# Kernel optimization log

Hardware: AMD Instinct MI355X
Metric: run time of the kernel (lower is better)

Reference implementation:

```python
import jax, jax.numpy as jnp
import numpy as np

N_NODES = 20000
N_EDGES = 640000
NODE_FEATURES = 8
PERIODS = 12
HIDDEN = 32


def _gcn_conv(x, src, dst, dinv, W, b):
    # GCNConv with added self-loops and symmetric normalization:
    # out = D^{-1/2}(A+I)D^{-1/2} (x W) + b
    xw = x @ W                                  # [N, H]
    norm = dinv[src] * dinv[dst]                # [E]
    agg = jax.ops.segment_sum(xw[src] * norm[:, None], dst, num_segments=x.shape[0])
    agg = agg + (dinv * dinv)[:, None] * xw     # self-loop contribution
    return agg + b


def _tgcn_cell(xt, src, dst, dinv, H, W_z, b_z, L_z, lb_z, W_r, b_r, L_r, lb_r, W_h, b_h, L_h, lb_h):
    # TGCN GRU-style cell (torch_geometric_temporal):
    Z = jax.nn.sigmoid(jnp.concatenate([_gcn_conv(xt, src, dst, dinv, W_z, b_z), H], axis=1) @ L_z + lb_z)
    R = jax.nn.sigmoid(jnp.concatenate([_gcn_conv(xt, src, dst, dinv, W_r, b_r), H], axis=1) @ L_r + lb_r)
    H_tilde = jnp.tanh(jnp.concatenate([_gcn_conv(xt, src, dst, dinv, W_h, b_h), H * R], axis=1) @ L_h + lb_h)
    return Z * H + (1.0 - Z) * H_tilde


def setup_inputs() -> dict:
    key = jax.random.key(0)
    ks = jax.random.split(key, 20)
    F, H, P = NODE_FEATURES, HIDDEN, PERIODS
    s = 0.1
    f32 = jnp.float32
    inp = {
        "x": jax.random.normal(ks[0], (N_NODES, F, P), f32),
        "edge_index": jax.random.randint(ks[1], (2, N_EDGES), 0, N_NODES, jnp.int32),
        # GCN gate conv weights (in_channels=F -> out_channels=H)
        "W_z": jax.random.normal(ks[2], (F, H), f32) * s, "b_z": jnp.zeros((H,), f32),
        "W_r": jax.random.normal(ks[3], (F, H), f32) * s, "b_r": jnp.zeros((H,), f32),
        "W_h": jax.random.normal(ks[4], (F, H), f32) * s, "b_h": jnp.zeros((H,), f32),
        # GRU linear layers: Linear(2H, H), stored as [2H, H]
        "L_z": jax.random.normal(ks[5], (2 * H, H), f32) * s, "lb_z": jnp.zeros((H,), f32),
        "L_r": jax.random.normal(ks[6], (2 * H, H), f32) * s, "lb_r": jnp.zeros((H,), f32),
        "L_h": jax.random.normal(ks[7], (2 * H, H), f32) * s, "lb_h": jnp.zeros((H,), f32),
        # attention over periods + final readout Linear(H, P)
        "attention": jax.random.uniform(ks[8], (P,), f32),
        "lin_W": jax.random.normal(ks[9], (H, P), f32) * s,
        "lin_b": jnp.zeros((P,), f32),
    }
    return inp


def reference(x, edge_index, W_z, b_z, W_r, b_r, W_h, b_h,
              L_z, lb_z, L_r, lb_r, L_h, lb_h, attention, lin_W, lin_b):
    N = x.shape[0]
    src, dst = edge_index[0], edge_index[1]
    # symmetric GCN normalization degrees (with self-loops)
    deg = jax.ops.segment_sum(jnp.ones((src.shape[0],), x.dtype), dst, num_segments=N) + 1.0
    dinv = jax.lax.rsqrt(deg)

    probs = jax.nn.softmax(attention)           # [P]
    H0 = jnp.zeros((N, W_z.shape[1]), x.dtype)  # A3TGCN passes H=None each period -> zeros
    xp = jnp.moveaxis(x, -1, 0)                 # [P, N, F]

    def step(acc, pt):
        xt, p = pt
        Hn = _tgcn_cell(xt, src, dst, dinv, H0,
                        W_z, b_z, L_z, lb_z, W_r, b_r, L_r, lb_r, W_h, b_h, L_h, lb_h)
        return acc + p * Hn, None

    H_accum, _ = jax.lax.scan(step, H0, (xp, probs))
    h = jax.nn.relu(H_accum)
    return h @ lin_W + lin_b                    # [N, P]
```

## Files before the change

### kernel.cpp

```cpp
#include <hip/hip_runtime.h>
#include <math.h>

#define NN 20000
#define NE 640000
#define FDIM 8
#define PDIM 12
#define HDIM 32
#define FP 96
#define CAP 96
#define CSTR 16

typedef _Float16 half4v __attribute__((ext_vector_type(4)));
typedef _Float16 half8v __attribute__((ext_vector_type(8)));

__global__ __launch_bounds__(256) void k_prep(
        int* __restrict__ cursor,
        const float* __restrict__ Wz, const float* __restrict__ bz,
        const float* __restrict__ Wh, const float* __restrict__ bh,
        const float* __restrict__ Lz, const float* __restrict__ lbz,
        const float* __restrict__ Lh, const float* __restrict__ lbh,
        const float* __restrict__ att,
        float* __restrict__ Mz, float* __restrict__ Mh,
        float* __restrict__ cz, float* __restrict__ ch,
        float* __restrict__ probs) {
    int tid = blockIdx.x * 256 + threadIdx.x;
    if (tid < NN * CSTR / 4) reinterpret_cast<int4*>(cursor)[tid] = make_int4(0, 0, 0, 0);

    if (blockIdx.x == 0) {
        int t = threadIdx.x;
        int f = t >> 5, h = t & 31;
        float mz = 0.f, mh = 0.f;
        for (int k = 0; k < HDIM; ++k) {
            mz += Wz[f * HDIM + k] * Lz[k * HDIM + h];
            mh += Wh[f * HDIM + k] * Lh[k * HDIM + h];
        }
        Mz[f * HDIM + h] = mz;
        Mh[f * HDIM + h] = mh;
        if (f == 0) {
            float a = lbz[h], b2 = lbh[h];
            for (int k = 0; k < HDIM; ++k) {
                a  += bz[k] * Lz[k * HDIM + h];
                b2 += bh[k] * Lh[k * HDIM + h];
            }
            cz[h] = a; ch[h] = b2;
        }
        if (t == 0) {
            float m = -1e30f;
            for (int p = 0; p < PDIM; ++p) m = fmaxf(m, att[p]);
            float e[PDIM]; float ss = 0.f;
            for (int p = 0; p < PDIM; ++p) { e[p] = expf(att[p] - m); ss += e[p]; }
            for (int p = 0; p < PDIM; ++p) probs[p] = e[p] / ss;
        }
    }
}

__global__ __launch_bounds__(256) void k_bucket(
        const int* __restrict__ src, const int* __restrict__ dst,
        int* __restrict__ cursor, unsigned short* __restrict__ ebuf) {
    int i = blockIdx.x * 256 + threadIdx.x;
    int s = src[i], d = dst[i];
    int p = atomicAdd(&cursor[d * CSTR], 1);
    if (p < CAP) ebuf[d * CAP + p] = (unsigned short)s;
}

__global__ __launch_bounds__(256) void k_xh(const float* __restrict__ x,
                                            const int* __restrict__ cursor,
                                            half8v* __restrict__ xh) {
    int idx = blockIdx.x * 256 + threadIdx.x;
    if (idx >= NN * (FP / 8)) return;
    int node = idx / (FP / 8);
    float dd = rsqrtf((float)cursor[node * CSTR] + 1.0f);
    const float4* xp = reinterpret_cast<const float4*>(x) + (size_t)idx * 2;
    float4 a = xp[0], b = xp[1];
    half8v h;
    h[0] = (_Float16)(dd * a.x); h[1] = (_Float16)(dd * a.y);
    h[2] = (_Float16)(dd * a.z); h[3] = (_Float16)(dd * a.w);
    h[4] = (_Float16)(dd * b.x); h[5] = (_Float16)(dd * b.y);
    h[6] = (_Float16)(dd * b.z); h[7] = (_Float16)(dd * b.w);
    xh[idx] = h;
}

__global__ __launch_bounds__(256) void k_gnode(
        const _Float16* __restrict__ xh, const int* __restrict__ cursor,
        const unsigned short* __restrict__ ebuf,
        const float* __restrict__ Mz, const float* __restrict__ Mh,
        const float* __restrict__ cz, const float* __restrict__ ch,
        const float* __restrict__ probs,
        const float* __restrict__ linW, const float* __restrict__ linb,
        float* __restrict__ out) {
    __shared__ float4 sx4[8 * 24];
    __shared__ float sh[8][HDIM];
    __shared__ float sprobs[PDIM];
    __shared__ unsigned short sle[8 * CAP];
    __shared__ int   scnt[8];
    __shared__ float sdd[8];

    int tid   = threadIdx.x;
    int node0 = blockIdx.x * 8;

    if (tid < PDIM) sprobs[tid] = probs[tid];
    if (tid < 8 * CAP / 4)
        reinterpret_cast<ushort4*>(sle)[tid] =
            reinterpret_cast<const ushort4*>(ebuf + (size_t)node0 * CAP)[tid];
    if (tid < 8) {
        int c = cursor[(node0 + tid) * CSTR];
        scnt[tid] = c < CAP ? c : CAP;
        sdd[tid]  = rsqrtf((float)c + 1.0f);
    }
    __syncthreads();

    int li   = tid >> 5;
    int lane = tid & 31;
    int node = node0 + li;

    if (lane < 24) {
        float dd = sdd[li];
        int e1 = scnt[li];
        const half4v* xh4 = reinterpret_cast<const half4v*>(xh);
        half4v hs = xh4[node * 24 + lane];
        float ax = (float)hs[0], ay = (float)hs[1];
        float az = (float)hs[2], aw = (float)hs[3];
        const unsigned short* eb = &sle[li * CAP];
        int j = 0;
        for (; j + 4 <= e1; j += 4) {
            ushort4 s4 = *reinterpret_cast<const ushort4*>(eb + j);
            half4v a0 = xh4[s4.x * 24 + lane], a1 = xh4[s4.y * 24 + lane];
            half4v a2 = xh4[s4.z * 24 + lane], a3 = xh4[s4.w * 24 + lane];
            ax += ((float)a0[0] + (float)a1[0]) + ((float)a2[0] + (float)a3[0]);
            ay += ((float)a0[1] + (float)a1[1]) + ((float)a2[1] + (float)a3[1]);
            az += ((float)a0[2] + (float)a1[2]) + ((float)a2[2] + (float)a3[2]);
            aw += ((float)a0[3] + (float)a1[3]) + ((float)a2[3] + (float)a3[3]);
        }
        for (; j < e1; ++j) {
            int s = eb[j];
            half4v a = xh4[s * 24 + lane];
            ax += (float)a[0]; ay += (float)a[1]; az += (float)a[2]; aw += (float)a[3];
        }
        float4 o;
        o.x = dd * ax; o.y = dd * ay; o.z = dd * az; o.w = dd * aw;
        sx4[li * 24 + lane] = o;
    }
    __syncthreads();

    int h = lane;
    float rMz[FDIM], rMh[FDIM];
#pragma unroll
    for (int f = 0; f < FDIM; ++f) {
        rMz[f] = Mz[f * HDIM + h];
        rMh[f] = Mh[f * HDIM + h];
    }
    float u[PDIM], v[PDIM];
    float c0 = cz[h], c1 = ch[h];
#pragma unroll
    for (int t = 0; t < PDIM; ++t) { u[t] = c0; v[t] = c1; }

    const float* sxf = reinterpret_cast<const float*>(&sx4[li * 24]);
#pragma unroll
    for (int f = 0; f < FDIM; ++f) {
        const float4 a = *reinterpret_cast<const float4*>(sxf + f * PDIM);
        const float4 b = *reinterpret_cast<const float4*>(sxf + f * PDIM + 4);
        const float4 c = *reinterpret_cast<const float4*>(sxf + f * PDIM + 8);
        float mz = rMz[f], mh = rMh[f];
        u[0] += a.x * mz; u[1]  += a.y * mz; u[2]  += a.z * mz; u[3]  += a.w * mz;
        u[4] += b.x * mz; u[5]  += b.y * mz; u[6]  += b.z * mz; u[7]  += b.w * mz;
        u[8] += c.x * mz; u[9]  += c.y * mz; u[10] += c.z * mz; u[11] += c.w * mz;
        v[0] += a.x * mh; v[1]  += a.y * mh; v[2]  += a.z * mh; v[3]  += a.w * mh;
        v[4] += b.x * mh; v[5]  += b.y * mh; v[6]  += b.z * mh; v[7]  += b.w * mh;
        v[8] += c.x * mh; v[9]  += c.y * mh; v[10] += c.z * mh; v[11] += c.w * mh;
    }

    float accum = 0.f;
#pragma unroll
    for (int t = 0; t < PDIM; ++t) {
        float omz = 1.f / (1.f + __expf(u[t]));
        float th  = 1.f - 2.f / (__expf(2.f * v[t]) + 1.f);
        accum += sprobs[t] * omz * th;
    }
    sh[li][h] = fmaxf(accum, 0.f);
    __builtin_amdgcn_wave_barrier();

    if (h < PDIM) {
        float o = linb[h];
#pragma unroll
        for (int k = 0; k < HDIM; ++k) o += sh[li][k] * linW[k * PDIM + h];
        out[(size_t)node * PDIM + h] = o;
    }
}

static inline size_t al256(size_t x) { return (x + 255) & ~(size_t)255; }

extern "C" void kernel_launch(void* const* d_in, const int* in_sizes, int n_in,
                              void* d_out, int out_size, void* d_ws, size_t ws_size,
                              hipStream_t stream) {
    const float* x    = (const float*)d_in[0];
    const int*   ei   = (const int*)d_in[1];
    const float* Wz   = (const float*)d_in[2];
    const float* bz   = (const float*)d_in[3];
    const float* Wh   = (const float*)d_in[6];
    const float* bh   = (const float*)d_in[7];
    const float* Lz   = (const float*)d_in[8];
    const float* lbz  = (const float*)d_in[9];
    const float* Lh   = (const float*)d_in[12];
    const float* lbh  = (const float*)d_in[13];
    const float* att  = (const float*)d_in[14];
    const float* linW = (const float*)d_in[15];
    const float* linb = (const float*)d_in[16];
    float* out = (float*)d_out;

    const int* src = ei;
    const int* dst = ei + NE;

    char* w = (char*)d_ws;
    size_t o = 0;
    int*            cursor = (int*)(w + o);            o += al256((size_t)NN * CSTR * 4);
    unsigned short* ebuf   = (unsigned short*)(w + o); o += al256((size_t)NN * CAP * 2);
    _Float16*       xh     = (_Float16*)(w + o);       o += al256((size_t)NN * FP * 2);
    float*          Mz     = (float*)(w + o);          o += al256((size_t)FDIM * HDIM * 4);
    float*          Mh     = (float*)(w + o);          o += al256((size_t)FDIM * HDIM * 4);
    float*          czp    = (float*)(w + o);          o += al256((size_t)HDIM * 4);
    float*          chp    = (float*)(w + o);          o += al256((size_t)HDIM * 4);
    float*          probs  = (float*)(w + o);          o += al256((size_t)PDIM * 4);

    const int B = 256;
    k_prep<<<(NN * CSTR / 4 + B - 1) / B, B, 0, stream>>>(cursor,
                                                          Wz, bz, Wh, bh,
                                                          Lz, lbz, Lh, lbh, att,
                                                          Mz, Mh, czp, chp, probs);
    k_bucket<<<NE / B, B, 0, stream>>>(src, dst, cursor, ebuf);
    k_xh<<<(NN * (FP / 8) + B - 1) / B, B, 0, stream>>>(x, cursor, (half8v*)xh);
    k_gnode<<<NN / 8, B, 0, stream>>>(xh, cursor, ebuf,
                                      Mz, Mh, czp, chp, probs, linW, linb, out);
}
```

Before: 73.87 us.

## Co-locate per-node edge counter and source list in one row buffer

```diff
diff --git a/kernel.cpp b/kernel.cpp
--- a/kernel.cpp
+++ b/kernel.cpp
@@ -7,14 +7,14 @@
 #define PDIM 12
 #define HDIM 32
 #define FP 96
-#define CAP 96
-#define CSTR 16
+#define CAPS 124
+#define ROWU 64
 
 typedef _Float16 half4v __attribute__((ext_vector_type(4)));
 typedef _Float16 half8v __attribute__((ext_vector_type(8)));
 
 __global__ __launch_bounds__(256) void k_prep(
-        int* __restrict__ cursor,
+        uint4* __restrict__ rowbuf4,
         const float* __restrict__ Wz, const float* __restrict__ bz,
         const float* __restrict__ Wh, const float* __restrict__ bh,
         const float* __restrict__ Lz, const float* __restrict__ lbz,
@@ -24,7 +24,7 @@
         float* __restrict__ cz, float* __restrict__ ch,
         float* __restrict__ probs) {
     int tid = blockIdx.x * 256 + threadIdx.x;
-    if (tid < NN * CSTR / 4) reinterpret_cast<int4*>(cursor)[tid] = make_int4(0, 0, 0, 0);
+    if (tid < NN * ROWU / 4) rowbuf4[tid] = make_uint4(0, 0, 0, 0);
 
     if (blockIdx.x == 0) {
         int t = threadIdx.x;
@@ -56,20 +56,22 @@
 
 __global__ __launch_bounds__(256) void k_bucket(
         const int* __restrict__ src, const int* __restrict__ dst,
-        int* __restrict__ cursor, unsigned short* __restrict__ ebuf) {
+        unsigned int* __restrict__ rowbuf) {
     int i = blockIdx.x * 256 + threadIdx.x;
     int s = src[i], d = dst[i];
-    int p = atomicAdd(&cursor[d * CSTR], 1);
-    if (p < CAP) ebuf[d * CAP + p] = (unsigned short)s;
+    int p = atomicAdd((int*)(rowbuf + (size_t)d * ROWU), 1);
+    if (p < CAPS)
+        reinterpret_cast<unsigned short*>(rowbuf)[(size_t)d * (ROWU * 2) + 4 + p] =
+            (unsigned short)s;
 }
 
 __global__ __launch_bounds__(256) void k_xh(const float* __restrict__ x,
-                                            const int* __restrict__ cursor,
+                                            const unsigned int* __restrict__ rowbuf,
                                             half8v* __restrict__ xh) {
     int idx = blockIdx.x * 256 + threadIdx.x;
     if (idx >= NN * (FP / 8)) return;
     int node = idx / (FP / 8);
-    float dd = rsqrtf((float)cursor[node * CSTR] + 1.0f);
+    float dd = rsqrtf((float)rowbuf[(size_t)node * ROWU] + 1.0f);
     const float4* xp = reinterpret_cast<const float4*>(x) + (size_t)idx * 2;
     float4 a = xp[0], b = xp[1];
     half8v h;
@@ -81,49 +83,59 @@
 }
 
 __global__ __launch_bounds__(256) void k_gnode(
-        const _Float16* __restrict__ xh, const int* __restrict__ cursor,
-        const unsigned short* __restrict__ ebuf,
+        const _Float16* __restrict__ xh, const unsigned int* __restrict__ rowbuf,
         const float* __restrict__ Mz, const float* __restrict__ Mh,
         const float* __restrict__ cz, const float* __restrict__ ch,
         const float* __restrict__ probs,
         const float* __restrict__ linW, const float* __restrict__ linb,
         float* __restrict__ out) {
+    __shared__ uint4  srow4[8][16];
     __shared__ float4 sx4[8 * 24];
-    __shared__ float sh[8][HDIM];
-    __shared__ float sprobs[PDIM];
-    __shared__ unsigned short sle[8 * CAP];
-    __shared__ int   scnt[8];
-    __shared__ float sdd[8];
+    __shared__ float  sh[8][HDIM];
+    __shared__ float  sprobs[PDIM];
 
     int tid   = threadIdx.x;
     int node0 = blockIdx.x * 8;
 
     if (tid < PDIM) sprobs[tid] = probs[tid];
-    if (tid < 8 * CAP / 4)
-        reinterpret_cast<ushort4*>(sle)[tid] =
-            reinterpret_cast<const ushort4*>(ebuf + (size_t)node0 * CAP)[tid];
-    if (tid < 8) {
-        int c = cursor[(node0 + tid) * CSTR];
-        scnt[tid] = c < CAP ? c : CAP;
-        sdd[tid]  = rsqrtf((float)c + 1.0f);
-    }
+    if (tid < 128)
+        reinterpret_cast<uint4*>(srow4)[tid] =
+            reinterpret_cast<const uint4*>(rowbuf)[(size_t)node0 * (ROWU / 4) + tid];
     __syncthreads();
 
     int li   = tid >> 5;
     int lane = tid & 31;
     int node = node0 + li;
 
+    int cnt = reinterpret_cast<const unsigned int*>(&srow4[li][0])[0];
+    int e1  = cnt < CAPS ? cnt : CAPS;
+    float dd = rsqrtf((float)cnt + 1.0f);
+    const unsigned short* sr = reinterpret_cast<const unsigned short*>(&srow4[li][0]);
+
     if (lane < 24) {
-        float dd = sdd[li];
-        int e1 = scnt[li];
         const half4v* xh4 = reinterpret_cast<const half4v*>(xh);
         half4v hs = xh4[node * 24 + lane];
         float ax = (float)hs[0], ay = (float)hs[1];
         float az = (float)hs[2], aw = (float)hs[3];
-        const unsigned short* eb = &sle[li * CAP];
         int j = 0;
+        for (; j + 8 <= e1; j += 8) {
+            ushort4 sA = *reinterpret_cast<const ushort4*>(sr + 4 + j);
+            ushort4 sB = *reinterpret_cast<const ushort4*>(sr + 4 + j + 4);
+            half4v a0 = xh4[sA.x * 24 + lane], a1 = xh4[sA.y * 24 + lane];
+            half4v a2 = xh4[sA.z * 24 + lane], a3 = xh4[sA.w * 24 + lane];
+            half4v a4 = xh4[sB.x * 24 + lane], a5 = xh4[sB.y * 24 + lane];
+            half4v a6 = xh4[sB.z * 24 + lane], a7 = xh4[sB.w * 24 + lane];
+            ax += (((float)a0[0] + (float)a1[0]) + ((float)a2[0] + (float)a3[0]))
+                + (((float)a4[0] + (float)a5[0]) + ((float)a6[0] + (float)a7[0]));
+            ay += (((float)a0[1] + (float)a1[1]) + ((float)a2[1] + (float)a3[1]))
+                + (((float)a4[1] + (float)a5[1]) + ((float)a6[1] + (float)a7[1]));
+            az += (((float)a0[2] + (float)a1[2]) + ((float)a2[2] + (float)a3[2]))
+                + (((float)a4[2] + (float)a5[2]) + ((float)a6[2] + (float)a7[2]));
+            aw += (((float)a0[3] + (float)a1[3]) + ((float)a2[3] + (float)a3[3]))
+                + (((float)a4[3] + (float)a5[3]) + ((float)a6[3] + (float)a7[3]));
+        }
         for (; j + 4 <= e1; j += 4) {
-            ushort4 s4 = *reinterpret_cast<const ushort4*>(eb + j);
+            ushort4 s4 = *reinterpret_cast<const ushort4*>(sr + 4 + j);
             half4v a0 = xh4[s4.x * 24 + lane], a1 = xh4[s4.y * 24 + lane];
             half4v a2 = xh4[s4.z * 24 + lane], a3 = xh4[s4.w * 24 + lane];
             ax += ((float)a0[0] + (float)a1[0]) + ((float)a2[0] + (float)a3[0]);
@@ -132,7 +144,7 @@
             aw += ((float)a0[3] + (float)a1[3]) + ((float)a2[3] + (float)a3[3]);
         }
         for (; j < e1; ++j) {
-            int s = eb[j];
+            int s = sr[4 + j];
             half4v a = xh4[s * 24 + lane];
             ax += (float)a[0]; ay += (float)a[1]; az += (float)a[2]; aw += (float)a[3];
         }
@@ -212,22 +224,21 @@
 
     char* w = (char*)d_ws;
     size_t o = 0;
-    int*            cursor = (int*)(w + o);            o += al256((size_t)NN * CSTR * 4);
-    unsigned short* ebuf   = (unsigned short*)(w + o); o += al256((size_t)NN * CAP * 2);
-    _Float16*       xh     = (_Float16*)(w + o);       o += al256((size_t)NN * FP * 2);
-    float*          Mz     = (float*)(w + o);          o += al256((size_t)FDIM * HDIM * 4);
-    float*          Mh     = (float*)(w + o);          o += al256((size_t)FDIM * HDIM * 4);
-    float*          czp    = (float*)(w + o);          o += al256((size_t)HDIM * 4);
-    float*          chp    = (float*)(w + o);          o += al256((size_t)HDIM * 4);
-    float*          probs  = (float*)(w + o);          o += al256((size_t)PDIM * 4);
+    unsigned int* rowbuf = (unsigned int*)(w + o); o += al256((size_t)NN * ROWU * 4);
+    _Float16*     xh     = (_Float16*)(w + o);     o += al256((size_t)NN * FP * 2);
+    float*        Mz     = (float*)(w + o);        o += al256((size_t)FDIM * HDIM * 4);
+    float*        Mh     = (float*)(w + o);        o += al256((size_t)FDIM * HDIM * 4);
+    float*        czp    = (float*)(w + o);        o += al256((size_t)HDIM * 4);
+    float*        chp    = (float*)(w + o);        o += al256((size_t)HDIM * 4);
+    float*        probs  = (float*)(w + o);        o += al256((size_t)PDIM * 4);
 
     const int B = 256;
-    k_prep<<<(NN * CSTR / 4 + B - 1) / B, B, 0, stream>>>(cursor,
+    k_prep<<<(NN * ROWU / 4 + B - 1) / B, B, 0, stream>>>((uint4*)rowbuf,
                                                           Wz, bz, Wh, bh,
                                                           Lz, lbz, Lh, lbh, att,
                                                           Mz, Mh, czp, chp, probs);
-    k_bucket<<<NE / B, B, 0, stream>>>(src, dst, cursor, ebuf);
-    k_xh<<<(NN * (FP / 8) + B - 1) / B, B, 0, stream>>>(x, cursor, (half8v*)xh);
-    k_gnode<<<NN / 8, B, 0, stream>>>(xh, cursor, ebuf,
+    k_bucket<<<NE / B, B, 0, stream>>>(src, dst, rowbuf);
+    k_xh<<<(NN * (FP / 8) + B - 1) / B, B, 0, stream>>>(x, rowbuf, (half8v*)xh);
+    k_gnode<<<NN / 8, B, 0, stream>>>(xh, rowbuf,
                                       Mz, Mh, czp, chp, probs, linW, linb, out);
 }
```

Measured after the change: 83.12 us. 1.13x slower.

## Replace global-atomic edge bucketing with chunked LDS histogram, scan and placement

Applied to the files above, without the earlier changes.

```diff
diff --git a/kernel.cpp b/kernel.cpp
--- a/kernel.cpp
+++ b/kernel.cpp
@@ -8,13 +8,32 @@
 #define HDIM 32
 #define FP 96
 #define CAP 96
-#define CSTR 16
+#define CHK 256
+#define ECH (NE / CHK)
+#define NP (NN / 2)
 
 typedef _Float16 half4v __attribute__((ext_vector_type(4)));
 typedef _Float16 half8v __attribute__((ext_vector_type(8)));
 
-__global__ __launch_bounds__(256) void k_prep(
-        int* __restrict__ cursor,
+__global__ __launch_bounds__(256) void k_hist(const int* __restrict__ dst,
+                                              unsigned int* __restrict__ hT) {
+    __shared__ unsigned int h32[NP];
+    int c = blockIdx.x, tid = threadIdx.x;
+    for (int i = tid; i < NP; i += 256) h32[i] = 0u;
+    __syncthreads();
+    const int* db = dst + c * ECH;
+    for (int e = tid; e < ECH; e += 256) {
+        int d = db[e];
+        atomicAdd(&h32[d >> 1], (d & 1) ? 65536u : 1u);
+    }
+    __syncthreads();
+    unsigned int* row = hT + (size_t)c * NP;
+    for (int i = tid; i < NP; i += 256) row[i] = h32[i];
+}
+
+__global__ __launch_bounds__(256) void k_scan(
+        unsigned int* __restrict__ hT, unsigned int* __restrict__ degp,
+        float2* __restrict__ dinv2,
         const float* __restrict__ Wz, const float* __restrict__ bz,
         const float* __restrict__ Wh, const float* __restrict__ bh,
         const float* __restrict__ Lz, const float* __restrict__ lbz,
@@ -23,12 +42,24 @@
         float* __restrict__ Mz, float* __restrict__ Mh,
         float* __restrict__ cz, float* __restrict__ ch,
         float* __restrict__ probs) {
-    int tid = blockIdx.x * 256 + threadIdx.x;
-    if (tid < NN * CSTR / 4) reinterpret_cast<int4*>(cursor)[tid] = make_int4(0, 0, 0, 0);
+    int t = blockIdx.x * 256 + threadIdx.x;
+    if (t < NP) {
+        unsigned run_lo = 0, run_hi = 0;
+        unsigned int* col = hT + t;
+#pragma unroll 8
+        for (int c = 0; c < CHK; ++c) {
+            unsigned v = col[(size_t)c * NP];
+            col[(size_t)c * NP] = run_lo | (run_hi << 16);
+            run_lo += v & 0xffffu;
+            run_hi += v >> 16;
+        }
+        degp[t] = run_lo | (run_hi << 16);
+        dinv2[t] = make_float2(rsqrtf((float)run_lo + 1.f), rsqrtf((float)run_hi + 1.f));
+    }
 
     if (blockIdx.x == 0) {
-        int t = threadIdx.x;
-        int f = t >> 5, h = t & 31;
+        int tt = threadIdx.x;
+        int f = tt >> 5, h = tt & 31;
         float mz = 0.f, mh = 0.f;
         for (int k = 0; k < HDIM; ++k) {
             mz += Wz[f * HDIM + k] * Lz[k * HDIM + h];
@@ -44,7 +75,7 @@
             }
             cz[h] = a; ch[h] = b2;
         }
-        if (t == 0) {
+        if (tt == 0) {
             float m = -1e30f;
             for (int p = 0; p < PDIM; ++p) m = fmaxf(m, att[p]);
             float e[PDIM]; float ss = 0.f;
@@ -54,22 +85,31 @@
     }
 }
 
-__global__ __launch_bounds__(256) void k_bucket(
+__global__ __launch_bounds__(256) void k_place(
         const int* __restrict__ src, const int* __restrict__ dst,
-        int* __restrict__ cursor, unsigned short* __restrict__ ebuf) {
-    int i = blockIdx.x * 256 + threadIdx.x;
-    int s = src[i], d = dst[i];
-    int p = atomicAdd(&cursor[d * CSTR], 1);
-    if (p < CAP) ebuf[d * CAP + p] = (unsigned short)s;
+        const unsigned int* __restrict__ hT, unsigned short* __restrict__ ebuf) {
+    __shared__ unsigned int cur[NP];
+    int c = blockIdx.x, tid = threadIdx.x;
+    const unsigned int* row = hT + (size_t)c * NP;
+    for (int i = tid; i < NP; i += 256) cur[i] = row[i];
+    __syncthreads();
+    const int* sb = src + c * ECH;
+    const int* db = dst + c * ECH;
+    for (int e = tid; e < ECH; e += 256) {
+        int d = db[e], s = sb[e];
+        unsigned old = atomicAdd(&cur[d >> 1], (d & 1) ? 65536u : 1u);
+        unsigned slot = (d & 1) ? (old >> 16) : (old & 0xffffu);
+        if (slot < CAP) ebuf[(size_t)d * CAP + slot] = (unsigned short)s;
+    }
 }
 
 __global__ __launch_bounds__(256) void k_xh(const float* __restrict__ x,
-                                            const int* __restrict__ cursor,
+                                            const float* __restrict__ dinv,
                                             half8v* __restrict__ xh) {
     int idx = blockIdx.x * 256 + threadIdx.x;
     if (idx >= NN * (FP / 8)) return;
     int node = idx / (FP / 8);
-    float dd = rsqrtf((float)cursor[node * CSTR] + 1.0f);
+    float dd = dinv[node];
     const float4* xp = reinterpret_cast<const float4*>(x) + (size_t)idx * 2;
     float4 a = xp[0], b = xp[1];
     half8v h;
@@ -81,7 +121,7 @@
 }
 
 __global__ __launch_bounds__(256) void k_gnode(
-        const _Float16* __restrict__ xh, const int* __restrict__ cursor,
+        const _Float16* __restrict__ xh, const unsigned short* __restrict__ deg16,
         const unsigned short* __restrict__ ebuf,
         const float* __restrict__ Mz, const float* __restrict__ Mh,
         const float* __restrict__ cz, const float* __restrict__ ch,
@@ -103,7 +143,7 @@
         reinterpret_cast<ushort4*>(sle)[tid] =
             reinterpret_cast<const ushort4*>(ebuf + (size_t)node0 * CAP)[tid];
     if (tid < 8) {
-        int c = cursor[(node0 + tid) * CSTR];
+        int c = deg16[node0 + tid];
         scnt[tid] = c < CAP ? c : CAP;
         sdd[tid]  = rsqrtf((float)c + 1.0f);
     }
@@ -212,22 +252,26 @@
 
     char* w = (char*)d_ws;
     size_t o = 0;
-    int*            cursor = (int*)(w + o);            o += al256((size_t)NN * CSTR * 4);
-    unsigned short* ebuf   = (unsigned short*)(w + o); o += al256((size_t)NN * CAP * 2);
-    _Float16*       xh     = (_Float16*)(w + o);       o += al256((size_t)NN * FP * 2);
-    float*          Mz     = (float*)(w + o);          o += al256((size_t)FDIM * HDIM * 4);
-    float*          Mh     = (float*)(w + o);          o += al256((size_t)FDIM * HDIM * 4);
-    float*          czp    = (float*)(w + o);          o += al256((size_t)HDIM * 4);
-    float*          chp    = (float*)(w + o);          o += al256((size_t)HDIM * 4);
-    float*          probs  = (float*)(w + o);          o += al256((size_t)PDIM * 4);
+    unsigned int*   hT    = (unsigned int*)(w + o);   o += al256((size_t)CHK * NP * 4);
+    unsigned short* ebuf  = (unsigned short*)(w + o); o += al256((size_t)NN * CAP * 2);
+    _Float16*       xh    = (_Float16*)(w + o);       o += al256((size_t)NN * FP * 2);
+    unsigned int*   degp  = (unsigned int*)(w + o);   o += al256((size_t)NP * 4);
+    float2*         dinv2 = (float2*)(w + o);         o += al256((size_t)NP * 8);
+    float*          Mz    = (float*)(w + o);          o += al256((size_t)FDIM * HDIM * 4);
+    float*          Mh    = (float*)(w + o);          o += al256((size_t)FDIM * HDIM * 4);
+    float*          czp   = (float*)(w + o);          o += al256((size_t)HDIM * 4);
+    float*          chp   = (float*)(w + o);          o += al256((size_t)HDIM * 4);
+    float*          probs = (float*)(w + o);          o += al256((size_t)PDIM * 4);
 
     const int B = 256;
-    k_prep<<<(NN * CSTR / 4 + B - 1) / B, B, 0, stream>>>(cursor,
-                                                          Wz, bz, Wh, bh,
-                                                          Lz, lbz, Lh, lbh, att,
-                                                          Mz, Mh, czp, chp, probs);
-    k_bucket<<<NE / B, B, 0, stream>>>(src, dst, cursor, ebuf);
-    k_xh<<<(NN * (FP / 8) + B - 1) / B, B, 0, stream>>>(x, cursor, (half8v*)xh);
-    k_gnode<<<NN / 8, B, 0, stream>>>(xh, cursor, ebuf,
+    k_hist<<<CHK, B, 0, stream>>>(dst, hT);
+    k_scan<<<(NP + B - 1) / B, B, 0, stream>>>(hT, degp, dinv2,
+                                               Wz, bz, Wh, bh,
+                                               Lz, lbz, Lh, lbh, att,
+                                               Mz, Mh, czp, chp, probs);
+    k_place<<<CHK, B, 0, stream>>>(src, dst, hT, ebuf);
+    k_xh<<<(NN * (FP / 8) + B - 1) / B, B, 0, stream>>>(x, (const float*)dinv2,
+                                                        (half8v*)xh);
+    k_gnode<<<NN / 8, B, 0, stream>>>(xh, (const unsigned short*)degp, ebuf,
                                       Mz, Mh, czp, chp, probs, linW, linb, out);
 }
```

New measurement: 76.76 us. +3.9%, slower.
